# Optimization experiments

Hardware: AMD Instinct MI355X
Metric: run time of the kernel (lower is better)

The kernel has to match this reference:

```python
import jax, jax.numpy as jnp
import numpy as np
from jax import lax

M = 4      # signature truncation depth (init kwarg m)
D = 6      # path channel dimension
L = 100000 # path length


def _kron(a, b):
    # flat tensor product of two flattened tensor levels
    return (a[:, None] * b[None, :]).ravel()


def signature(x, m):
    """Truncated path signature of x (L, d) up to depth m, flat concat of levels.
    Matches iisignature.sig(x, m): output size d + d^2 + ... + d^m.
    Sequential Chen recursion over path increments via lax.scan."""
    d = x.shape[1]
    dx = x[1:] - x[:-1]  # (L-1, d) increments

    def step(S, v):
        # exp of the linear segment: e[k] = v^{(x)k} / k!
        e = [v]
        for k in range(2, m + 1):
            e.append(_kron(e[-1], v) / k)
        # Chen: S'^k = S^k + e^k + sum_{j=1}^{k-1} S^j (x) e^{k-j}
        newS = []
        for k in range(1, m + 1):
            t = S[k - 1] + e[k - 1]
            for j in range(1, k):
                t = t + _kron(S[j - 1], e[k - 1 - j])
            newS.append(t)
        return tuple(newS), None

    S0 = tuple(jnp.zeros((d ** k,), x.dtype) for k in range(1, m + 1))
    S, _ = lax.scan(step, S0, dx)
    return jnp.concatenate(S)  # (d + d^2 + ... + d^m,)


def setup_inputs() -> dict:
    key = jax.random.key(0)
    # build a realistic path: cumulative sum of small Gaussian increments
    steps = jax.random.normal(key, (L, D), dtype=jnp.float32) * 0.01
    x = jnp.cumsum(steps, axis=0)
    return {"x": x}


def reference(x) -> jnp.ndarray:
    return signature(x, M)
```

## Files before the change

### kernel.cpp

```cpp
#include <hip/hip_runtime.h>

#define SIGSZ 1554
#define PSTRIDE 1600
#define OFF4 0
#define OFF3 1296
#define OFF2 1512
#define OFF1 1548
#define MAXROWS 80

#define REP6(M) M(0) M(1) M(2) M(3) M(4) M(5)
#define REP6B(M, k) M(k, 0) M(k, 1) M(k, 2) M(k, 3) M(k, 4) M(k, 5)
#define REP36(M) \
  REP6B(M, 0) REP6B(M, 1) REP6B(M, 2) REP6B(M, 3) REP6B(M, 4) REP6B(M, 5)

__device__ __forceinline__ float sel6(int idx, float a0, float a1, float a2,
                                      float a3, float a4, float a5) {
  float r = a0;
  r = (idx == 1) ? a1 : r;
  r = (idx == 2) ? a2 : r;
  r = (idx == 3) ? a3 : r;
  r = (idx == 4) ? a4 : r;
  r = (idx == 5) ? a5 : r;
  return r;
}

__global__ __launch_bounds__(64, 1) void sig_chunk(const float* __restrict__ x,
                                                   float* __restrict__ out,
                                                   int n_inc, int chunk_len) {
  __shared__ float xs[MAXROWS * 6];
  const int c = blockIdx.x;
  const int p = threadIdx.x;
  const int t0 = c * chunk_len;
  int t1 = t0 + chunk_len; if (t1 > n_inc) t1 = n_inc;
  const int steps = (t1 > t0) ? (t1 - t0) : 0;
  const int pc = (p < 36) ? p : 35;
  const int i = pc / 6, j = pc % 6;
  const bool act = (p < 36);

  const int nfl = (steps > 0) ? (steps + 1) * 6 : 0;
  for (int idx = p; idx < nfl; idx += 64) xs[idx] = x[(size_t)t0 * 6 + idx];
  __syncthreads();

#define DECL_S4(k, l) float s4_##k##_##l = 0.f;
  REP36(DECL_S4)
#undef DECL_S4
#define DECL_S3(k) float s3_##k = 0.f;
  REP6(DECL_S3)
#undef DECL_S3
  float s1i = 0.f, s2 = 0.f;

  float cr0 = 0, cr1 = 0, cr2 = 0, cr3 = 0, cr4 = 0, cr5 = 0;
  float nr0 = 0, nr1 = 0, nr2 = 0, nr3 = 0, nr4 = 0, nr5 = 0;
  if (steps > 0) {
    const float2* q0 = (const float2*)(xs);
    float2 a0 = q0[0], b0 = q0[1], d0 = q0[2];
    cr0 = a0.x; cr1 = a0.y; cr2 = b0.x; cr3 = b0.y; cr4 = d0.x; cr5 = d0.y;
    const float2* q1 = (const float2*)(xs + 6);
    float2 a1 = q1[0], b1 = q1[1], d1 = q1[2];
    nr0 = a1.x; nr1 = a1.y; nr2 = b1.x; nr3 = b1.y; nr4 = d1.x; nr5 = d1.y;
  }

  for (int r = 0; r < steps; ++r) {
    const float v0 = nr0 - cr0, v1 = nr1 - cr1, v2 = nr2 - cr2;
    const float v3 = nr3 - cr3, v4 = nr4 - cr4, v5 = nr5 - cr5;

    int ro = r + 2; ro = (ro > steps) ? steps : ro;
    const float2* qp = (const float2*)(xs + ro * 6);
    const float2 pa = qp[0], pb = qp[1], pd = qp[2];

    const float vi = sel6(i, v0, v1, v2, v3, v4, v5);
    const float vj = sel6(j, v0, v1, v2, v3, v4, v5);
    const float aa = vi * vj;
    const float sv = s1i * vj;
    const float G2  = fmaf(aa, 1.f / 6.f,  fmaf(sv, 0.5f,      s2));
    const float in4 = fmaf(aa, 1.f / 24.f, fmaf(sv, 1.f / 6.f, s2 * 0.5f));
#define MKG(k)                                    \
    const float G_##k = fmaf(in4, v##k, s3_##k);  \
    s3_##k = fmaf(G2, v##k, s3_##k);
    REP6(MKG)
#undef MKG
#define UPD4(k, l) s4_##k##_##l = fmaf(G_##k, v##l, s4_##k##_##l);
    REP36(UPD4)
#undef UPD4
    s2 = fmaf(fmaf(vi, 0.5f, s1i), vj, s2);
    s1i += vi;

    cr0 = nr0; cr1 = nr1; cr2 = nr2; cr3 = nr3; cr4 = nr4; cr5 = nr5;
    nr0 = pa.x; nr1 = pa.y; nr2 = pb.x; nr3 = pb.y; nr4 = pd.x; nr5 = pd.y;
  }

  float* st = out + (size_t)c * PSTRIDE;
  if (act) {
    float4* o4 = (float4*)(st + OFF4 + pc * 36);
    float4 w;
    w.x = s4_0_0; w.y = s4_0_1; w.z = s4_0_2; w.w = s4_0_3; o4[0] = w;
    w.x = s4_0_4; w.y = s4_0_5; w.z = s4_1_0; w.w = s4_1_1; o4[1] = w;
    w.x = s4_1_2; w.y = s4_1_3; w.z = s4_1_4; w.w = s4_1_5; o4[2] = w;
    w.x = s4_2_0; w.y = s4_2_1; w.z = s4_2_2; w.w = s4_2_3; o4[3] = w;
    w.x = s4_2_4; w.y = s4_2_5; w.z = s4_3_0; w.w = s4_3_1; o4[4] = w;
    w.x = s4_3_2; w.y = s4_3_3; w.z = s4_3_4; w.w = s4_3_5; o4[5] = w;
    w.x = s4_4_0; w.y = s4_4_1; w.z = s4_4_2; w.w = s4_4_3; o4[6] = w;
    w.x = s4_4_4; w.y = s4_4_5; w.z = s4_5_0; w.w = s4_5_1; o4[7] = w;
    w.x = s4_5_2; w.y = s4_5_3; w.z = s4_5_4; w.w = s4_5_5; o4[8] = w;
#define ST3(k) st[OFF3 + pc * 6 + k] = s3_##k;
    REP6(ST3)
#undef ST3
    st[OFF2 + pc] = s2;
    if (j == 0) st[OFF1 + i] = s1i;
  }
}


#define DECLSET(S)                                                  \
  float S##b4_0, S##b4_1, S##b4_2, S##b4_3, S##b4_4, S##b4_5;       \
  float S##b3r_0, S##b3r_1, S##b3r_2, S##b3r_3, S##b3r_4, S##b3r_5; \
  float S##b2r_0, S##b2r_1, S##b2r_2, S##b2r_3, S##b2r_4, S##b2r_5; \
  float S##b1_0, S##b1_1, S##b1_2, S##b1_3, S##b1_4, S##b1_5;       \
  float S##b2ij, S##b2jk, S##b3ijk, S##b1k, S##b1j;

#define LOADSET(S, bp) {                                            \
  const float2* q4 = (const float2*)((bp) + oB4);                   \
  float2 u0 = q4[0], u1 = q4[1], u2 = q4[2];                        \
  S##b4_0 = u0.x; S##b4_1 = u0.y; S##b4_2 = u1.x;                   \
  S##b4_3 = u1.y; S##b4_4 = u2.x; S##b4_5 = u2.y;                   \
  const float2* q3 = (const float2*)((bp) + oB3r);                  \
  float2 w0 = q3[0], w1 = q3[1], w2 = q3[2];                        \
  S##b3r_0 = w0.x; S##b3r_1 = w0.y; S##b3r_2 = w1.x;                \
  S##b3r_3 = w1.y; S##b3r_4 = w2.x; S##b3r_5 = w2.y;                \
  const float2* q2 = (const float2*)((bp) + oB2r);                  \
  float2 y0 = q2[0], y1 = q2[1], y2 = q2[2];                        \
  S##b2r_0 = y0.x; S##b2r_1 = y0.y; S##b2r_2 = y1.x;                \
  S##b2r_3 = y1.y; S##b2r_4 = y2.x; S##b2r_5 = y2.y;                \
  const float2* q1 = (const float2*)((bp) + OFF1);                  \
  float2 z0 = q1[0], z1 = q1[1], z2 = q1[2];                        \
  S##b1_0 = z0.x; S##b1_1 = z0.y; S##b1_2 = z1.x;                   \
  S##b1_3 = z1.y; S##b1_4 = z2.x; S##b1_5 = z2.y;                   \
  S##b2ij = (bp)[oB2ij]; S##b2jk = (bp)[oB2jk];                     \
  S##b3ijk = (bp)[oB3ijk];                                          \
  S##b1k = (bp)[oB1k]; S##b1j = (bp)[oB1j];                         \
}

#define PROD(S) {                                                   \
  const float a1i = sel6(i_, a1_0, a1_1, a1_2, a1_3, a1_4, a1_5);   \
  a4_0 = fmaf(a3, S##b1_0, fmaf(a2, S##b2r_0,                       \
         fmaf(a1i, S##b3r_0, a4_0 + S##b4_0)));                     \
  a4_1 = fmaf(a3, S##b1_1, fmaf(a2, S##b2r_1,                       \
         fmaf(a1i, S##b3r_1, a4_1 + S##b4_1)));                     \
  a4_2 = fmaf(a3, S##b1_2, fmaf(a2, S##b2r_2,                       \
         fmaf(a1i, S##b3r_2, a4_2 + S##b4_2)));                     \
  a4_3 = fmaf(a3, S##b1_3, fmaf(a2, S##b2r_3,                       \
         fmaf(a1i, S##b3r_3, a4_3 + S##b4_3)));                     \
  a4_4 = fmaf(a3, S##b1_4, fmaf(a2, S##b2r_4,                       \
         fmaf(a1i, S##b3r_4, a4_4 + S##b4_4)));                     \
  a4_5 = fmaf(a3, S##b1_5, fmaf(a2, S##b2r_5,                       \
         fmaf(a1i, S##b3r_5, a4_5 + S##b4_5)));                     \
  a3 = fmaf(a2, S##b1k, fmaf(a1i, S##b2jk, a3 + S##b3ijk));         \
  a2 = fmaf(a1i, S##b1j, a2 + S##b2ij);                             \
  a1_0 += S##b1_0; a1_1 += S##b1_1; a1_2 += S##b1_2;                \
  a1_3 += S##b1_3; a1_4 += S##b1_4; a1_5 += S##b1_5;                \
}

__global__ __launch_bounds__(256, 1) void sig_combine(const float* __restrict__ in,
                                                      float* __restrict__ out,
                                                      int n_total, int group,
                                                      int final_out) {
  const int b = blockIdx.x;
  const int p = threadIdx.x;
  const int start = b * group;
  int end = start + group; if (end > n_total) end = n_total;
  const int tc = (p < 216) ? p : 215;
  const bool act = (p < 216);
  const int k_ = tc % 6;
  const int ij = tc / 6;
  const int j_ = ij % 6;
  const int i_ = ij / 6;

  const int oB4 = OFF4 + tc * 6;
  const int oB3r = OFF3 + (j_ * 6 + k_) * 6;
  const int oB2r = OFF2 + k_ * 6;
  const int oB2ij = OFF2 + ij;
  const int oB2jk = OFF2 + j_ * 6 + k_;
  const int oB3ijk = OFF3 + tc;
  const int oB1k = OFF1 + k_;
  const int oB1j = OFF1 + j_;

  const float* sp0 = in + (size_t)start * PSTRIDE;
  float a4_0, a4_1, a4_2, a4_3, a4_4, a4_5;
  {
    const float2* q4 = (const float2*)(sp0 + oB4);
    float2 u0 = q4[0], u1 = q4[1], u2 = q4[2];
    a4_0 = u0.x; a4_1 = u0.y; a4_2 = u1.x;
    a4_3 = u1.y; a4_4 = u2.x; a4_5 = u2.y;
  }
  float a3 = sp0[oB3ijk];
  float a2 = sp0[oB2ij];
  float a1_0, a1_1, a1_2, a1_3, a1_4, a1_5;
  {
    const float2* q1 = (const float2*)(sp0 + OFF1);
    float2 z0 = q1[0], z1 = q1[1], z2 = q1[2];
    a1_0 = z0.x; a1_1 = z0.y; a1_2 = z1.x;
    a1_3 = z1.y; a1_4 = z2.x; a1_5 = z2.y;
  }

  DECLSET(A)
  DECLSET(B)

  int s = start + 1;
  {
    const int sa = (s < end) ? s : (end - 1);
    LOADSET(A, in + (size_t)sa * PSTRIDE)
    const int sb = (s + 1 < end) ? (s + 1) : (end - 1);
    LOADSET(B, in + (size_t)sb * PSTRIDE)
  }
  while (s + 1 < end) {
    PROD(A)
    {
      const int sn = (s + 2 < end) ? (s + 2) : (end - 1);
      LOADSET(A, in + (size_t)sn * PSTRIDE)
    }
    PROD(B)
    {
      const int sn = (s + 3 < end) ? (s + 3) : (end - 1);
      LOADSET(B, in + (size_t)sn * PSTRIDE)
    }
    s += 2;
  }
  if (s < end) { PROD(A) }

  const float a1p = sel6(p, a1_0, a1_1, a1_2, a1_3, a1_4, a1_5);
  if (final_out) {
    float* o = out;
    if (act) {
      float2* o2 = (float2*)(o + 258 + tc * 6);
      float2 w;
      w.x = a4_0; w.y = a4_1; o2[0] = w;
      w.x = a4_2; w.y = a4_3; o2[1] = w;
      w.x = a4_4; w.y = a4_5; o2[2] = w;
      o[42 + tc] = a3;
      if (k_ == 0) o[6 + ij] = a2;
    }
    if (p < 6) o[p] = a1p;
  } else {
    float* st = out + (size_t)b * PSTRIDE;
    if (act) {
      float2* o2 = (float2*)(st + oB4);
      float2 w;
      w.x = a4_0; w.y = a4_1; o2[0] = w;
      w.x = a4_2; w.y = a4_3; o2[1] = w;
      w.x = a4_4; w.y = a4_5; o2[2] = w;
      st[oB3ijk] = a3;
      if (k_ == 0) st[oB2ij] = a2;
    }
    if (p < 6) st[OFF1 + p] = a1p;
  }
}

extern "C" void kernel_launch(void* const* d_in, const int* in_sizes, int n_in,
                              void* d_out, int out_size, void* d_ws, size_t ws_size,
                              hipStream_t stream) {
  const float* x = (const float*)d_in[0];
  const int Lrows = in_sizes[0] / 6;
  const int n_inc = Lrows - 1;

  int P = 2048;
  int chunk_len = (n_inc + P - 1) / P;
  if (chunk_len > MAXROWS - 1) {
    chunk_len = MAXROWS - 1;
    P = (n_inc + chunk_len - 1) / chunk_len;
  }

  float* ws0 = (float*)d_ws;
  float* ws1 = ws0 + (size_t)P * PSTRIDE;

  sig_chunk<<<P, 64, 0, stream>>>(x, ws0, n_inc, chunk_len);

  float* cur = ws0;
  float* other = ws1;
  int n = P;
  while (n > 1) {
    const int g = (n <= 16) ? n : 16;
    const int nb = (n + g - 1) / g;
    const int fin = (nb == 1);
    sig_combine<<<nb, 256, 0, stream>>>(cur, fin ? (float*)d_out : other, n, g, fin);
    float* t = cur; cur = other; other = t;
    n = nb;
  }
}
```

Measured before the change: 94.31 us.

## Retune chunk/combine sizes, triple-buffer combine loads, load vi/vj directly from LDS

Raises the maximum chunk length, halves the number of chunk blocks and widens the combine group, which changes how work is split between the chunk and tree-combine kernels (P=1024 gives chunk_len 98 and group 32). The chunk loop now reads the i/j path coordinates straight from shared memory instead of selecting them from the six registers with sel6, and is unrolled by two. The combine kernel moves from double to triple buffering of prefetched partial signatures, with a tail that handles the leftover A or B set. Together these aim to cut per-block overhead and the number of combine levels while keeping more loads in flight, at the cost of longer sequential chains per block, fewer blocks to fill the GPU, and more registers.

```diff
diff --git a/kernel.cpp b/kernel.cpp
--- a/kernel.cpp
+++ b/kernel.cpp
@@ -6,7 +6,7 @@
 #define OFF3 1296
 #define OFF2 1512
 #define OFF1 1548
-#define MAXROWS 80
+#define MAXROWS 100
 
 #define REP6(M) M(0) M(1) M(2) M(3) M(4) M(5)
 #define REP6B(M, k) M(k, 0) M(k, 1) M(k, 2) M(k, 3) M(k, 4) M(k, 5)
@@ -51,6 +51,7 @@
 
   float cr0 = 0, cr1 = 0, cr2 = 0, cr3 = 0, cr4 = 0, cr5 = 0;
   float nr0 = 0, nr1 = 0, nr2 = 0, nr3 = 0, nr4 = 0, nr5 = 0;
+  float xic = 0, xjc = 0, xin = 0, xjn = 0;
   if (steps > 0) {
     const float2* q0 = (const float2*)(xs);
     float2 a0 = q0[0], b0 = q0[1], d0 = q0[2];
@@ -58,18 +59,23 @@
     const float2* q1 = (const float2*)(xs + 6);
     float2 a1 = q1[0], b1 = q1[1], d1 = q1[2];
     nr0 = a1.x; nr1 = a1.y; nr2 = b1.x; nr3 = b1.y; nr4 = d1.x; nr5 = d1.y;
-  }
-
+    xic = xs[i]; xjc = xs[j];
+    xin = xs[6 + i]; xjn = xs[6 + j];
+  }
+
+#pragma unroll 2
   for (int r = 0; r < steps; ++r) {
     const float v0 = nr0 - cr0, v1 = nr1 - cr1, v2 = nr2 - cr2;
     const float v3 = nr3 - cr3, v4 = nr4 - cr4, v5 = nr5 - cr5;
+    const float vi = xin - xic;
+    const float vj = xjn - xjc;
 
     int ro = r + 2; ro = (ro > steps) ? steps : ro;
     const float2* qp = (const float2*)(xs + ro * 6);
     const float2 pa = qp[0], pb = qp[1], pd = qp[2];
-
-    const float vi = sel6(i, v0, v1, v2, v3, v4, v5);
-    const float vj = sel6(j, v0, v1, v2, v3, v4, v5);
+    const float xi2 = xs[ro * 6 + i];
+    const float xj2 = xs[ro * 6 + j];
+
     const float aa = vi * vj;
     const float sv = s1i * vj;
     const float G2  = fmaf(aa, 1.f / 6.f,  fmaf(sv, 0.5f,      s2));
@@ -87,6 +93,7 @@
 
     cr0 = nr0; cr1 = nr1; cr2 = nr2; cr3 = nr3; cr4 = nr4; cr5 = nr5;
     nr0 = pa.x; nr1 = pa.y; nr2 = pb.x; nr3 = pb.y; nr4 = pd.x; nr5 = pd.y;
+    xic = xin; xjc = xjn; xin = xi2; xjn = xj2;
   }
 
   float* st = out + (size_t)c * PSTRIDE;
@@ -204,28 +211,27 @@
 
   DECLSET(A)
   DECLSET(B)
-
+  DECLSET(C)
+
+#define CL(sx) ((sx) < end ? (sx) : (end - 1))
   int s = start + 1;
   {
-    const int sa = (s < end) ? s : (end - 1);
-    LOADSET(A, in + (size_t)sa * PSTRIDE)
-    const int sb = (s + 1 < end) ? (s + 1) : (end - 1);
-    LOADSET(B, in + (size_t)sb * PSTRIDE)
-  }
-  while (s + 1 < end) {
+    LOADSET(A, in + (size_t)CL(s) * PSTRIDE)
+    LOADSET(B, in + (size_t)CL(s + 1) * PSTRIDE)
+    LOADSET(C, in + (size_t)CL(s + 2) * PSTRIDE)
+  }
+  while (s + 2 < end) {
     PROD(A)
-    {
-      const int sn = (s + 2 < end) ? (s + 2) : (end - 1);
-      LOADSET(A, in + (size_t)sn * PSTRIDE)
-    }
+    LOADSET(A, in + (size_t)CL(s + 3) * PSTRIDE)
     PROD(B)
-    {
-      const int sn = (s + 3 < end) ? (s + 3) : (end - 1);
-      LOADSET(B, in + (size_t)sn * PSTRIDE)
-    }
-    s += 2;
+    LOADSET(B, in + (size_t)CL(s + 4) * PSTRIDE)
+    PROD(C)
+    LOADSET(C, in + (size_t)CL(s + 5) * PSTRIDE)
+    s += 3;
   }
   if (s < end) { PROD(A) }
+  if (s + 1 < end) { PROD(B) }
+#undef CL
 
   const float a1p = sel6(p, a1_0, a1_1, a1_2, a1_3, a1_4, a1_5);
   if (final_out) {
@@ -262,7 +268,7 @@
   const int Lrows = in_sizes[0] / 6;
   const int n_inc = Lrows - 1;
 
-  int P = 2048;
+  int P = 1024;
   int chunk_len = (n_inc + P - 1) / P;
   if (chunk_len > MAXROWS - 1) {
     chunk_len = MAXROWS - 1;
@@ -278,7 +284,7 @@
   float* other = ws1;
   int n = P;
   while (n > 1) {
-    const int g = (n <= 16) ? n : 16;
+    const int g = (n <= 32) ? n : 32;
     const int nb = (n + g - 1) / g;
     const int fin = (nb == 1);
     sig_combine<<<nb, 256, 0, stream>>>(cur, fin ? (float*)d_out : other, n, g, fin);
```

Result: slower. 96.94 us (+2.8%).

## Fuse chunk signatures and tree combine into one kernel with atomic last-block reduction

Applied to the files above, without the earlier changes.

Merges the per-chunk signature kernel and the multi-launch combine tree into a single kernel. Each block runs four wavefronts over four sub-chunks, combines their states in shared memory, then uses atomic counters so the last-arriving block of each 32-block group (and then the last group) does the higher-level Chen combines. Increments are precomputed once in shared memory, and the per-step index selects are replaced by direct shared loads. This removes several kernel launches and global round trips, but adds a memset, threadfences and a serial tail where the final combines run in only a few blocks.

```diff
diff --git a/kernel.cpp b/kernel.cpp
--- a/kernel.cpp
+++ b/kernel.cpp
@@ -6,7 +6,11 @@
 #define OFF3 1296
 #define OFF2 1512
 #define OFF1 1548
-#define MAXROWS 80
+#define SSTRIDE 1560
+#define MAXCL 32
+#define NBMAX 2048
+#define NGMAX 64
+#define GSZ 32
 
 #define REP6(M) M(0) M(1) M(2) M(3) M(4) M(5)
 #define REP6B(M, k) M(k, 0) M(k, 1) M(k, 2) M(k, 3) M(k, 4) M(k, 5)
@@ -24,99 +28,12 @@
   return r;
 }
 
-__global__ __launch_bounds__(64, 1) void sig_chunk(const float* __restrict__ x,
-                                                   float* __restrict__ out,
-                                                   int n_inc, int chunk_len) {
-  __shared__ float xs[MAXROWS * 6];
-  const int c = blockIdx.x;
-  const int p = threadIdx.x;
-  const int t0 = c * chunk_len;
-  int t1 = t0 + chunk_len; if (t1 > n_inc) t1 = n_inc;
-  const int steps = (t1 > t0) ? (t1 - t0) : 0;
-  const int pc = (p < 36) ? p : 35;
-  const int i = pc / 6, j = pc % 6;
-  const bool act = (p < 36);
-
-  const int nfl = (steps > 0) ? (steps + 1) * 6 : 0;
-  for (int idx = p; idx < nfl; idx += 64) xs[idx] = x[(size_t)t0 * 6 + idx];
-  __syncthreads();
-
-#define DECL_S4(k, l) float s4_##k##_##l = 0.f;
-  REP36(DECL_S4)
-#undef DECL_S4
-#define DECL_S3(k) float s3_##k = 0.f;
-  REP6(DECL_S3)
-#undef DECL_S3
-  float s1i = 0.f, s2 = 0.f;
-
-  float cr0 = 0, cr1 = 0, cr2 = 0, cr3 = 0, cr4 = 0, cr5 = 0;
-  float nr0 = 0, nr1 = 0, nr2 = 0, nr3 = 0, nr4 = 0, nr5 = 0;
-  if (steps > 0) {
-    const float2* q0 = (const float2*)(xs);
-    float2 a0 = q0[0], b0 = q0[1], d0 = q0[2];
-    cr0 = a0.x; cr1 = a0.y; cr2 = b0.x; cr3 = b0.y; cr4 = d0.x; cr5 = d0.y;
-    const float2* q1 = (const float2*)(xs + 6);
-    float2 a1 = q1[0], b1 = q1[1], d1 = q1[2];
-    nr0 = a1.x; nr1 = a1.y; nr2 = b1.x; nr3 = b1.y; nr4 = d1.x; nr5 = d1.y;
-  }
-
-  for (int r = 0; r < steps; ++r) {
-    const float v0 = nr0 - cr0, v1 = nr1 - cr1, v2 = nr2 - cr2;
-    const float v3 = nr3 - cr3, v4 = nr4 - cr4, v5 = nr5 - cr5;
-
-    int ro = r + 2; ro = (ro > steps) ? steps : ro;
-    const float2* qp = (const float2*)(xs + ro * 6);
-    const float2 pa = qp[0], pb = qp[1], pd = qp[2];
-
-    const float vi = sel6(i, v0, v1, v2, v3, v4, v5);
-    const float vj = sel6(j, v0, v1, v2, v3, v4, v5);
-    const float aa = vi * vj;
-    const float sv = s1i * vj;
-    const float G2  = fmaf(aa, 1.f / 6.f,  fmaf(sv, 0.5f,      s2));
-    const float in4 = fmaf(aa, 1.f / 24.f, fmaf(sv, 1.f / 6.f, s2 * 0.5f));
-#define MKG(k)                                    \
-    const float G_##k = fmaf(in4, v##k, s3_##k);  \
-    s3_##k = fmaf(G2, v##k, s3_##k);
-    REP6(MKG)
-#undef MKG
-#define UPD4(k, l) s4_##k##_##l = fmaf(G_##k, v##l, s4_##k##_##l);
-    REP36(UPD4)
-#undef UPD4
-    s2 = fmaf(fmaf(vi, 0.5f, s1i), vj, s2);
-    s1i += vi;
-
-    cr0 = nr0; cr1 = nr1; cr2 = nr2; cr3 = nr3; cr4 = nr4; cr5 = nr5;
-    nr0 = pa.x; nr1 = pa.y; nr2 = pb.x; nr3 = pb.y; nr4 = pd.x; nr5 = pd.y;
-  }
-
-  float* st = out + (size_t)c * PSTRIDE;
-  if (act) {
-    float4* o4 = (float4*)(st + OFF4 + pc * 36);
-    float4 w;
-    w.x = s4_0_0; w.y = s4_0_1; w.z = s4_0_2; w.w = s4_0_3; o4[0] = w;
-    w.x = s4_0_4; w.y = s4_0_5; w.z = s4_1_0; w.w = s4_1_1; o4[1] = w;
-    w.x = s4_1_2; w.y = s4_1_3; w.z = s4_1_4; w.w = s4_1_5; o4[2] = w;
-    w.x = s4_2_0; w.y = s4_2_1; w.z = s4_2_2; w.w = s4_2_3; o4[3] = w;
-    w.x = s4_2_4; w.y = s4_2_5; w.z = s4_3_0; w.w = s4_3_1; o4[4] = w;
-    w.x = s4_3_2; w.y = s4_3_3; w.z = s4_3_4; w.w = s4_3_5; o4[5] = w;
-    w.x = s4_4_0; w.y = s4_4_1; w.z = s4_4_2; w.w = s4_4_3; o4[6] = w;
-    w.x = s4_4_4; w.y = s4_4_5; w.z = s4_5_0; w.w = s4_5_1; o4[7] = w;
-    w.x = s4_5_2; w.y = s4_5_3; w.z = s4_5_4; w.w = s4_5_5; o4[8] = w;
-#define ST3(k) st[OFF3 + pc * 6 + k] = s3_##k;
-    REP6(ST3)
-#undef ST3
-    st[OFF2 + pc] = s2;
-    if (j == 0) st[OFF1 + i] = s1i;
-  }
-}
-
-
 #define DECLSET(S)                                                  \
   float S##b4_0, S##b4_1, S##b4_2, S##b4_3, S##b4_4, S##b4_5;       \
   float S##b3r_0, S##b3r_1, S##b3r_2, S##b3r_3, S##b3r_4, S##b3r_5; \
   float S##b2r_0, S##b2r_1, S##b2r_2, S##b2r_3, S##b2r_4, S##b2r_5; \
   float S##b1_0, S##b1_1, S##b1_2, S##b1_3, S##b1_4, S##b1_5;       \
-  float S##b2ij, S##b2jk, S##b3ijk, S##b1k, S##b1j;
+  float S##b2ij, S##b2jk, S##b3ijk, S##b1k, S##b1j, S##b1i;
 
 #define LOADSET(S, bp) {                                            \
   const float2* q4 = (const float2*)((bp) + oB4);                   \
@@ -137,11 +54,10 @@
   S##b1_3 = z1.y; S##b1_4 = z2.x; S##b1_5 = z2.y;                   \
   S##b2ij = (bp)[oB2ij]; S##b2jk = (bp)[oB2jk];                     \
   S##b3ijk = (bp)[oB3ijk];                                          \
-  S##b1k = (bp)[oB1k]; S##b1j = (bp)[oB1j];                         \
+  S##b1k = (bp)[oB1k]; S##b1j = (bp)[oB1j]; S##b1i = (bp)[oB1i];    \
 }
 
 #define PROD(S) {                                                   \
-  const float a1i = sel6(i_, a1_0, a1_1, a1_2, a1_3, a1_4, a1_5);   \
   a4_0 = fmaf(a3, S##b1_0, fmaf(a2, S##b2r_0,                       \
          fmaf(a1i, S##b3r_0, a4_0 + S##b4_0)));                     \
   a4_1 = fmaf(a3, S##b1_1, fmaf(a2, S##b2r_1,                       \
@@ -156,102 +72,238 @@
          fmaf(a1i, S##b3r_5, a4_5 + S##b4_5)));                     \
   a3 = fmaf(a2, S##b1k, fmaf(a1i, S##b2jk, a3 + S##b3ijk));         \
   a2 = fmaf(a1i, S##b1j, a2 + S##b2ij);                             \
+  a1i += S##b1i;                                                    \
   a1_0 += S##b1_0; a1_1 += S##b1_1; a1_2 += S##b1_2;                \
   a1_3 += S##b1_3; a1_4 += S##b1_4; a1_5 += S##b1_5;                \
 }
 
-__global__ __launch_bounds__(256, 1) void sig_combine(const float* __restrict__ in,
-                                                      float* __restrict__ out,
-                                                      int n_total, int group,
-                                                      int final_out) {
+#define INITA(bp) {                                                 \
+  const float2* q4 = (const float2*)((bp) + oB4);                   \
+  float2 u0 = q4[0], u1 = q4[1], u2 = q4[2];                        \
+  a4_0 = u0.x; a4_1 = u0.y; a4_2 = u1.x;                            \
+  a4_3 = u1.y; a4_4 = u2.x; a4_5 = u2.y;                            \
+  a3 = (bp)[oB3ijk]; a2 = (bp)[oB2ij];                              \
+  const float2* q1 = (const float2*)((bp) + OFF1);                  \
+  float2 z0 = q1[0], z1 = q1[1], z2 = q1[2];                        \
+  a1_0 = z0.x; a1_1 = z0.y; a1_2 = z1.x;                            \
+  a1_3 = z1.y; a1_4 = z2.x; a1_5 = z2.y;                            \
+  a1i = (bp)[oB1i];                                                 \
+}
+
+#define GCLAMP(sx, n) (((sx) < (n)) ? (sx) : ((n) - 1))
+#define GLOOP(base, n) {                                            \
+  int s_ = 1;                                                       \
+  LOADSET(A, (base) + (size_t)GCLAMP(1, (n)) * PSTRIDE)             \
+  LOADSET(B, (base) + (size_t)GCLAMP(2, (n)) * PSTRIDE)             \
+  while (s_ + 1 < (n)) {                                            \
+    PROD(A)                                                         \
+    LOADSET(A, (base) + (size_t)GCLAMP(s_ + 2, (n)) * PSTRIDE)      \
+    PROD(B)                                                         \
+    LOADSET(B, (base) + (size_t)GCLAMP(s_ + 3, (n)) * PSTRIDE)      \
+    s_ += 2;                                                        \
+  }                                                                 \
+  if (s_ < (n)) { PROD(A) }                                         \
+}
+
+#define STORE_STATE(dst) {                                          \
+  if (act2) {                                                       \
+    float2* o2 = (float2*)((dst) + oB4);                            \
+    float2 wv_;                                                     \
+    wv_.x = a4_0; wv_.y = a4_1; o2[0] = wv_;                        \
+    wv_.x = a4_2; wv_.y = a4_3; o2[1] = wv_;                        \
+    wv_.x = a4_4; wv_.y = a4_5; o2[2] = wv_;                        \
+    (dst)[oB3ijk] = a3;                                             \
+    if (k2 == 0) (dst)[oB2ij] = a2;                                 \
+  }                                                                 \
+  if (tid < 6) (dst)[OFF1 + tid] = sel6(tid, a1_0, a1_1, a1_2,      \
+                                        a1_3, a1_4, a1_5);          \
+}
+
+__global__ __launch_bounds__(256) void sig_fused(
+    const float* __restrict__ x, float* __restrict__ ws1,
+    float* __restrict__ ws2, int* __restrict__ ctr,
+    float* __restrict__ out, int n_inc, int CL, int NB, int NG1) {
+  __shared__ __align__(16) float xls[(4 * MAXCL + 1) * 6];
+  __shared__ __align__(16) float vls[4 * MAXCL * 6];
+  __shared__ __align__(16) float Sb[4 * SSTRIDE];
+  __shared__ int flag;
+
   const int b = blockIdx.x;
-  const int p = threadIdx.x;
-  const int start = b * group;
-  int end = start + group; if (end > n_total) end = n_total;
-  const int tc = (p < 216) ? p : 215;
-  const bool act = (p < 216);
-  const int k_ = tc % 6;
-  const int ij = tc / 6;
-  const int j_ = ij % 6;
-  const int i_ = ij / 6;
-
+  const int tid = threadIdx.x;
+  const int w = tid >> 6;
+  const int lane = tid & 63;
+
+  const int t0b = b * 4 * CL;
+  const int xtot = (4 * CL + 1) * 6;
+  const int xlim = (n_inc + 1) * 6 - t0b * 6;
+  for (int idx = tid; idx < xtot; idx += 256)
+    xls[idx] = (idx < xlim) ? x[(size_t)t0b * 6 + idx] : 0.f;
+  __syncthreads();
+  const int remi = n_inc - t0b;
+  const int vlim = (remi > 0) ? remi * 6 : 0;
+  const int vtot = 4 * CL * 6;
+  for (int idx = tid; idx < vtot; idx += 256)
+    vls[idx] = (idx < vlim) ? (xls[idx + 6] - xls[idx]) : 0.f;
+  __syncthreads();
+
+  const int pc = (lane < 36) ? lane : 35;
+  const int i_ = pc / 6, j_ = pc % 6;
+
+#define DECL_S4(k, l) float s4_##k##_##l = 0.f;
+  REP36(DECL_S4)
+#undef DECL_S4
+#define DECL_S3(k) float s3_##k = 0.f;
+  REP6(DECL_S3)
+#undef DECL_S3
+  float s1i = 0.f, s2 = 0.f;
+
+  const float* vp = vls + w * CL * 6;
+  float va0, va1, va2, va3, va4, va5, vb0, vb1, vb2, vb3, vb4, vb5;
+  {
+    const float2* q0 = (const float2*)(vp);
+    float2 a0 = q0[0], b0 = q0[1], d0 = q0[2];
+    va0 = a0.x; va1 = a0.y; va2 = b0.x; va3 = b0.y; va4 = d0.x; va5 = d0.y;
+    const float2* q1 = (const float2*)(vp + 6);
+    float2 a1q = q1[0], b1q = q1[1], d1q = q1[2];
+    vb0 = a1q.x; vb1 = a1q.y; vb2 = b1q.x; vb3 = b1q.y; vb4 = d1q.x; vb5 = d1q.y;
+  }
+  float viA = vp[i_], vjA = vp[j_];
+  float viB = vp[6 + i_], vjB = vp[6 + j_];
+
+#pragma unroll 2
+  for (int r = 0; r < CL; ++r) {
+    int rn = r + 2; rn = (rn > CL - 1) ? (CL - 1) : rn;
+    const float2* qp = (const float2*)(vp + rn * 6);
+    const float2 pa = qp[0], pb = qp[1], pd = qp[2];
+    const float viC = vp[rn * 6 + i_];
+    const float vjC = vp[rn * 6 + j_];
+
+    const float v0 = va0, v1 = va1, v2 = va2;
+    const float v3 = va3, v4 = va4, v5 = va5;
+    const float vi = viA, vj = vjA;
+
+    const float aa = vi * vj;
+    const float sv = s1i * vj;
+    const float G2  = fmaf(aa, 1.f / 6.f,  fmaf(sv, 0.5f,      s2));
+    const float in4 = fmaf(aa, 1.f / 24.f, fmaf(sv, 1.f / 6.f, s2 * 0.5f));
+#define MKG(k)                                    \
+    const float G_##k = fmaf(in4, v##k, s3_##k);  \
+    s3_##k = fmaf(G2, v##k, s3_##k);
+    REP6(MKG)
+#undef MKG
+#define UPD4(k, l) s4_##k##_##l = fmaf(G_##k, v##l, s4_##k##_##l);
+    REP36(UPD4)
+#undef UPD4
+    s2 = fmaf(fmaf(vi, 0.5f, s1i), vj, s2);
+    s1i += vi;
+
+    va0 = vb0; va1 = vb1; va2 = vb2; va3 = vb3; va4 = vb4; va5 = vb5;
+    vb0 = pa.x; vb1 = pa.y; vb2 = pb.x; vb3 = pb.y; vb4 = pd.x; vb5 = pd.y;
+    viA = viB; vjA = vjB; viB = viC; vjB = vjC;
+  }
+
+  {
+    float* st = Sb + w * SSTRIDE;
+    if (lane < 36) {
+      float4* o4 = (float4*)(st + OFF4 + pc * 36);
+      float4 wv;
+      wv.x = s4_0_0; wv.y = s4_0_1; wv.z = s4_0_2; wv.w = s4_0_3; o4[0] = wv;
+      wv.x = s4_0_4; wv.y = s4_0_5; wv.z = s4_1_0; wv.w = s4_1_1; o4[1] = wv;
+      wv.x = s4_1_2; wv.y = s4_1_3; wv.z = s4_1_4; wv.w = s4_1_5; o4[2] = wv;
+      wv.x = s4_2_0; wv.y = s4_2_1; wv.z = s4_2_2; wv.w = s4_2_3; o4[3] = wv;
+      wv.x = s4_2_4; wv.y = s4_2_5; wv.z = s4_3_0; wv.w = s4_3_1; o4[4] = wv;
+      wv.x = s4_3_2; wv.y = s4_3_3; wv.z = s4_3_4; wv.w = s4_3_5; o4[5] = wv;
+      wv.x = s4_4_0; wv.y = s4_4_1; wv.z = s4_4_2; wv.w = s4_4_3; o4[6] = wv;
+      wv.x = s4_4_4; wv.y = s4_4_5; wv.z = s4_5_0; wv.w = s4_5_1; o4[7] = wv;
+      wv.x = s4_5_2; wv.y = s4_5_3; wv.z = s4_5_4; wv.w = s4_5_5; o4[8] = wv;
+#define ST3(k) st[OFF3 + pc * 6 + k] = s3_##k;
+      REP6(ST3)
+#undef ST3
+      st[OFF2 + pc] = s2;
+      if (j_ == 0) st[OFF1 + i_] = s1i;
+    }
+  }
+  __syncthreads();
+
+  const int tc = (tid < 216) ? tid : 215;
+  const bool act2 = (tid < 216);
+  const int k2 = tc % 6;
+  const int ij2 = tc / 6;
+  const int j2 = ij2 % 6;
+  const int i2 = ij2 / 6;
   const int oB4 = OFF4 + tc * 6;
-  const int oB3r = OFF3 + (j_ * 6 + k_) * 6;
-  const int oB2r = OFF2 + k_ * 6;
-  const int oB2ij = OFF2 + ij;
-  const int oB2jk = OFF2 + j_ * 6 + k_;
+  const int oB3r = OFF3 + (j2 * 6 + k2) * 6;
+  const int oB2r = OFF2 + k2 * 6;
+  const int oB2ij = OFF2 + ij2;
+  const int oB2jk = OFF2 + j2 * 6 + k2;
   const int oB3ijk = OFF3 + tc;
-  const int oB1k = OFF1 + k_;
-  const int oB1j = OFF1 + j_;
-
-  const float* sp0 = in + (size_t)start * PSTRIDE;
-  float a4_0, a4_1, a4_2, a4_3, a4_4, a4_5;
-  {
-    const float2* q4 = (const float2*)(sp0 + oB4);
-    float2 u0 = q4[0], u1 = q4[1], u2 = q4[2];
-    a4_0 = u0.x; a4_1 = u0.y; a4_2 = u1.x;
-    a4_3 = u1.y; a4_4 = u2.x; a4_5 = u2.y;
-  }
-  float a3 = sp0[oB3ijk];
-  float a2 = sp0[oB2ij];
-  float a1_0, a1_1, a1_2, a1_3, a1_4, a1_5;
-  {
-    const float2* q1 = (const float2*)(sp0 + OFF1);
-    float2 z0 = q1[0], z1 = q1[1], z2 = q1[2];
-    a1_0 = z0.x; a1_1 = z0.y; a1_2 = z1.x;
-    a1_3 = z1.y; a1_4 = z2.x; a1_5 = z2.y;
-  }
-
+  const int oB1k = OFF1 + k2;
+  const int oB1j = OFF1 + j2;
+  const int oB1i = OFF1 + i2;
+
+  float a4_0, a4_1, a4_2, a4_3, a4_4, a4_5, a3, a2;
+  float a1_0, a1_1, a1_2, a1_3, a1_4, a1_5, a1i;
   DECLSET(A)
   DECLSET(B)
 
-  int s = start + 1;
-  {
-    const int sa = (s < end) ? s : (end - 1);
-    LOADSET(A, in + (size_t)sa * PSTRIDE)
-    const int sb = (s + 1 < end) ? (s + 1) : (end - 1);
-    LOADSET(B, in + (size_t)sb * PSTRIDE)
-  }
-  while (s + 1 < end) {
-    PROD(A)
-    {
-      const int sn = (s + 2 < end) ? (s + 2) : (end - 1);
-      LOADSET(A, in + (size_t)sn * PSTRIDE)
+  {
+    const float* s0 = Sb;
+    INITA(s0)
+    LOADSET(A, Sb + 1 * SSTRIDE) PROD(A)
+    LOADSET(A, Sb + 2 * SSTRIDE) PROD(A)
+    LOADSET(A, Sb + 3 * SSTRIDE) PROD(A)
+  }
+
+  {
+    float* dst = ws1 + (size_t)b * PSTRIDE;
+    STORE_STATE(dst)
+  }
+  __threadfence();
+  __syncthreads();
+
+  const int g = b / GSZ;
+  const int gbase = g * GSZ;
+  int gcnt = NB - gbase; if (gcnt > GSZ) gcnt = GSZ;
+  if (tid == 0) {
+    int ret = atomicAdd(&ctr[g], 1);
+    flag = (ret == gcnt - 1) ? 1 : 0;
+  }
+  __syncthreads();
+  if (!flag) return;
+  __threadfence();
+
+  {
+    const float* base = ws1 + (size_t)gbase * PSTRIDE;
+    INITA(base)
+    GLOOP(base, gcnt)
+    float* dst = ws2 + (size_t)g * PSTRIDE;
+    STORE_STATE(dst)
+  }
+  __threadfence();
+  __syncthreads();
+
+  if (tid == 0) {
+    int ret = atomicAdd(&ctr[NG1], 1);
+    flag = (ret == NG1 - 1) ? 1 : 0;
+  }
+  __syncthreads();
+  if (!flag) return;
+  __threadfence();
+
+  {
+    const float* base = ws2;
+    INITA(base)
+    GLOOP(base, NG1)
+    if (act2) {
+      float2* o2 = (float2*)(out + 258 + tc * 6);
+      float2 wv;
+      wv.x = a4_0; wv.y = a4_1; o2[0] = wv;
+      wv.x = a4_2; wv.y = a4_3; o2[1] = wv;
+      wv.x = a4_4; wv.y = a4_5; o2[2] = wv;
+      out[42 + tc] = a3;
+      if (k2 == 0) out[6 + ij2] = a2;
     }
-    PROD(B)
-    {
-      const int sn = (s + 3 < end) ? (s + 3) : (end - 1);
-      LOADSET(B, in + (size_t)sn * PSTRIDE)
-    }
-    s += 2;
-  }
-  if (s < end) { PROD(A) }
-
-  const float a1p = sel6(p, a1_0, a1_1, a1_2, a1_3, a1_4, a1_5);
-  if (final_out) {
-    float* o = out;
-    if (act) {
-      float2* o2 = (float2*)(o + 258 + tc * 6);
-      float2 w;
-      w.x = a4_0; w.y = a4_1; o2[0] = w;
-      w.x = a4_2; w.y = a4_3; o2[1] = w;
-      w.x = a4_4; w.y = a4_5; o2[2] = w;
-      o[42 + tc] = a3;
-      if (k_ == 0) o[6 + ij] = a2;
-    }
-    if (p < 6) o[p] = a1p;
-  } else {
-    float* st = out + (size_t)b * PSTRIDE;
-    if (act) {
-      float2* o2 = (float2*)(st + oB4);
-      float2 w;
-      w.x = a4_0; w.y = a4_1; o2[0] = w;
-      w.x = a4_2; w.y = a4_3; o2[1] = w;
-      w.x = a4_4; w.y = a4_5; o2[2] = w;
-      st[oB3ijk] = a3;
-      if (k_ == 0) st[oB2ij] = a2;
-    }
-    if (p < 6) st[OFF1 + p] = a1p;
+    if (tid < 6) out[tid] = sel6(tid, a1_0, a1_1, a1_2, a1_3, a1_4, a1_5);
   }
 }
 
@@ -262,27 +314,18 @@
   const int Lrows = in_sizes[0] / 6;
   const int n_inc = Lrows - 1;
 
-  int P = 2048;
-  int chunk_len = (n_inc + P - 1) / P;
-  if (chunk_len > MAXROWS - 1) {
-    chunk_len = MAXROWS - 1;
-    P = (n_inc + chunk_len - 1) / chunk_len;
-  }
-
-  float* ws0 = (float*)d_ws;
-  float* ws1 = ws0 + (size_t)P * PSTRIDE;
-
-  sig_chunk<<<P, 64, 0, stream>>>(x, ws0, n_inc, chunk_len);
-
-  float* cur = ws0;
-  float* other = ws1;
-  int n = P;
-  while (n > 1) {
-    const int g = (n <= 16) ? n : 16;
-    const int nb = (n + g - 1) / g;
-    const int fin = (nb == 1);
-    sig_combine<<<nb, 256, 0, stream>>>(cur, fin ? (float*)d_out : other, n, g, fin);
-    float* t = cur; cur = other; other = t;
-    n = nb;
-  }
-}
+  int CL = (n_inc + 4096 - 1) / 4096;
+  if (CL < 1) CL = 1;
+  if (CL > MAXCL) CL = MAXCL;
+  int NB = (n_inc + 4 * CL - 1) / (4 * CL);
+  if (NB > NBMAX) NB = NBMAX;
+  const int NG1 = (NB + GSZ - 1) / GSZ;
+
+  float* ws1 = (float*)d_ws;
+  float* ws2 = ws1 + (size_t)NBMAX * PSTRIDE;
+  int* ctr = (int*)(ws2 + (size_t)NGMAX * PSTRIDE);
+
+  hipMemsetAsync(ctr, 0, (size_t)(NG1 + 1) * sizeof(int), stream);
+  sig_fused<<<NB, 256, 0, stream>>>(x, ws1, ws2, ctr, (float*)d_out,
+                                    n_inc, CL, NB, NG1);
+}
```

Measured after the change: 234.1 us. 2.48x slower.
